# Performance work log

Measured on AMD Instinct MI355X. Metric: run time of the kernel, lower is better.

Reference implementation:

```python
import jax, jax.numpy as jnp
import numpy as np
from jax import lax

B, C, H, W = 8, 1024, 64, 48
A = 9  # anchors per location

def _conv(x, w, b, pad):
    y = lax.conv_general_dilated(x, w, (1, 1), pad,
                                 dimension_numbers=('NCHW', 'OIHW', 'NCHW'))
    return y + b[None, :, None, None]

def setup_inputs() -> dict:
    key = jax.random.key(0)
    ks = jax.random.split(key, 12)
    base_feat = jax.random.normal(ks[0], (B, C, H, W), dtype=jnp.float32)
    W_conv = jax.random.normal(ks[1], (512, C, 3, 3), dtype=jnp.float32) * 0.01
    b_conv = jnp.zeros((512,), jnp.float32)
    W_cls = jax.random.normal(ks[2], (18, 512, 1, 1), dtype=jnp.float32) * 0.01
    b_cls = jnp.zeros((18,), jnp.float32)
    W_bbox = jax.random.normal(ks[3], (36, 512, 1, 1), dtype=jnp.float32) * 0.01
    b_bbox = jnp.zeros((36,), jnp.float32)
    # anchor-target-layer outputs (data-dependent assignment) provided as inputs
    rpn_label = (jax.random.randint(ks[4], (B, A * H * W), 0, 3) - 1).astype(jnp.int32)  # {-1,0,1}
    rpn_bbox_targets = jax.random.normal(ks[5], (B, 36, H, W), dtype=jnp.float32) * 0.1
    rpn_bbox_inside_weights = (jax.random.uniform(ks[6], (B, 36, H, W)) < 0.25).astype(jnp.float32)
    rpn_bbox_outside_weights = jax.random.uniform(ks[7], (B, 36, H, W), dtype=jnp.float32) * 0.01
    return {"base_feat": base_feat, "W_conv": W_conv, "b_conv": b_conv,
            "W_cls": W_cls, "b_cls": b_cls, "W_bbox": W_bbox, "b_bbox": b_bbox,
            "rpn_label": rpn_label, "rpn_bbox_targets": rpn_bbox_targets,
            "rpn_bbox_inside_weights": rpn_bbox_inside_weights,
            "rpn_bbox_outside_weights": rpn_bbox_outside_weights}

def reference(base_feat, W_conv, b_conv, W_cls, b_cls, W_bbox, b_bbox,
              rpn_label, rpn_bbox_targets, rpn_bbox_inside_weights,
              rpn_bbox_outside_weights):
    # RPN head: 3x3 conv + relu, then 1x1 cls / bbox heads
    rpn_conv1 = jax.nn.relu(_conv(base_feat, W_conv, b_conv, ((1, 1), (1, 1))))
    cls_score = _conv(rpn_conv1, W_cls, b_cls, ((0, 0), (0, 0)))   # [B,18,H,W]
    bbox_pred = _conv(rpn_conv1, W_bbox, b_bbox, ((0, 0), (0, 0)))  # [B,36,H,W]
    # reshape to [B,2,A*H,W], softmax over the 2-way fg/bg axis, reshape back
    score_rs = cls_score.reshape(B, 2, A * H, W)
    prob_rs = jax.nn.softmax(score_rs, axis=1)
    rpn_cls_prob = prob_rs.reshape(B, 18, H, W)
    # classification loss: permute(0,2,3,1).view(-1,2), keep labels != -1
    logits = score_rs.transpose(0, 2, 3, 1).reshape(-1, 2)
    label = rpn_label.reshape(-1)
    valid = (label != -1).astype(logits.dtype)
    logp = jax.nn.log_softmax(logits, axis=-1)
    lbl = jnp.clip(label, 0, 1)
    nll = -jnp.take_along_axis(logp, lbl[:, None].astype(jnp.int32), axis=1)[:, 0]
    rpn_loss_cls = jnp.sum(nll * valid) / jnp.maximum(jnp.sum(valid), 1.0)
    # smooth-L1 box loss, sigma=3, summed over dims [1,2,3], mean over batch
    sigma2 = 9.0
    in_diff = rpn_bbox_inside_weights * (bbox_pred - rpn_bbox_targets)
    abs_d = jnp.abs(in_diff)
    sign = lax.stop_gradient((abs_d < 1.0 / sigma2).astype(abs_d.dtype))
    in_loss = in_diff * in_diff * (sigma2 / 2.0) * sign + (abs_d - 0.5 / sigma2) * (1.0 - sign)
    rpn_loss_box = jnp.mean(jnp.sum(rpn_bbox_outside_weights * in_loss, axis=(1, 2, 3)))
    return rpn_cls_prob, bbox_pred, rpn_loss_cls, rpn_loss_box
```

## Files before the change

### kernel.cpp

```cpp
#include <hip/hip_runtime.h>
#include <stdint.h>

#define B_    8
#define CIN   1024
#define H_    64
#define W_    48
#define OC    512
#define HW    3072
#define NPOS  24576
#define K9    9216
#define HP    66
#define WP    50

typedef __attribute__((ext_vector_type(8))) __bf16 bf16x8;
typedef __attribute__((ext_vector_type(4))) float  float4_t;
typedef __attribute__((ext_vector_type(4))) unsigned short ushort4_t;
typedef __attribute__((ext_vector_type(8))) int int8v;
typedef __attribute__((ext_vector_type(4))) int int4v;

__device__ __forceinline__ unsigned short f2bf(float x) {
  union { float f; unsigned u; } v; v.f = x;
  unsigned r = v.u + 0x7FFFu + ((v.u >> 16) & 1u);
  return (unsigned short)(r >> 16);
}

__device__ __forceinline__ unsigned int pack4_fp8(float a, float b, float c, float d) {
  int w = __builtin_amdgcn_cvt_pk_fp8_f32(a, b, 0, false);
  w = __builtin_amdgcn_cvt_pk_fp8_f32(c, d, w, true);
  return (unsigned int)w;
}

__device__ __forceinline__ void async16(const void* g, void* l) {
  __builtin_amdgcn_global_load_lds(
      (const __attribute__((address_space(1))) unsigned int*)g,
      (__attribute__((address_space(3))) unsigned int*)l, 16, 0, 0);
}

__device__ __forceinline__ float wave_sum(float v) {
  for (int o = 32; o > 0; o >>= 1) v += __shfl_down(v, o, 64);
  return v;
}

__global__ void prep_fused(const float* __restrict__ x, const float* __restrict__ Wc,
                           const float* __restrict__ Wcls, const float* __restrict__ Wbb,
                           unsigned char* __restrict__ xt, unsigned char* __restrict__ Wa,
                           unsigned short* __restrict__ Wh, float* __restrict__ accbuf) {
  __shared__ float smem[9216];
  int bid = blockIdx.x, t = threadIdx.x;
  if (bid < 4096) {
    int cx = bid & 7, h = (bid >> 3) & 63, b = bid >> 9;
    float* tile = smem;
    const float* src = x + ((long)(b * CIN + cx * 128) * H_ + h) * W_;
    for (int it = 0; it < 6; ++it) {
      int e = it * 256 + t;
      int cl = e / 12, w4 = e % 12;
      float4_t v = *(const float4_t*)&src[(long)cl * HW + w4 * 4];
      int base = cl * 49 + w4 * 4;
      tile[base] = v.x; tile[base + 1] = v.y; tile[base + 2] = v.z; tile[base + 3] = v.w;
    }
    __syncthreads();
    unsigned char* dst = xt + ((long)(b * HP + h + 1) * WP + 1) * CIN + cx * 128;
    for (int it = 0; it < 6; ++it) {
      int e = it * 256 + t;
      int w = e >> 5, g = e & 31;
      float v0 = tile[(g * 4 + 0) * 49 + w] * 16.f;
      float v1 = tile[(g * 4 + 1) * 49 + w] * 16.f;
      float v2 = tile[(g * 4 + 2) * 49 + w] * 16.f;
      float v3 = tile[(g * 4 + 3) * 49 + w] * 16.f;
      *(unsigned int*)&dst[(long)w * CIN + g * 4] = pack4_fp8(v0, v1, v2, v3);
    }
  } else if (bid < 4608) {
    int o = bid - 4096;
    float* lw = smem;
    const float* src = Wc + (long)o * K9;
    for (int i = 0; i < 9; ++i)
      *(float4_t*)&lw[i * 1024 + t * 4] = *(const float4_t*)&src[i * 1024 + t * 4];
    __syncthreads();
    unsigned char* dst = Wa + (long)o * K9;
    int c = t * 4;
    for (int off = 0; off < 9; ++off) {
      float v0 = lw[(c + 0) * 9 + off] * 512.f;
      float v1 = lw[(c + 1) * 9 + off] * 512.f;
      float v2 = lw[(c + 2) * 9 + off] * 512.f;
      float v3 = lw[(c + 3) * 9 + off] * 512.f;
      *(unsigned int*)&dst[off * 1024 + c] = pack4_fp8(v0, v1, v2, v3);
    }
  } else if (bid < 4640) {
    int e = (bid - 4608) * 1024 + t * 4;
    int m = e >> 9, c = e & 511;
    float v0 = 0.f, v1 = 0.f, v2 = 0.f, v3 = 0.f;
    if (m < 18) {
      const float* s = Wcls + m * 512 + c;
      v0 = s[0]; v1 = s[1]; v2 = s[2]; v3 = s[3];
    } else if (m < 54) {
      const float* s = Wbb + (m - 18) * 512 + c;
      v0 = s[0]; v1 = s[1]; v2 = s[2]; v3 = s[3];
    }
    ushort4_t pk; pk.x = f2bf(v0); pk.y = f2bf(v1); pk.z = f2bf(v2); pk.w = f2bf(v3);
    *(ushort4_t*)&Wh[e] = pk;
    if (bid == 4608 && t < 4) accbuf[t] = 0.f;
  } else {
    int bid2 = bid - 4640;
    int b = bid2 / 66, h = bid2 % 66;
    unsigned char* base = xt + (long)(b * 66 + h) * 50 * 1024;
    int4v z = {};
    if (h == 0 || h == 65) {
      for (int i = t; i < 3200; i += 256) *(int4v*)(base + (long)i * 16) = z;
    } else if (t < 128) {
      int which = t >> 6, off = t & 63;
      *(int4v*)(base + (long)which * 49 * 1024 + (long)off * 16) = z;
    }
  }
}

#define BKF 128
__global__ __launch_bounds__(256, 2)
void conv_gemm(const unsigned char* __restrict__ Wa, const unsigned char* __restrict__ xt,
               const float* __restrict__ bias, unsigned short* __restrict__ conv1) {
  __shared__ unsigned char As[128 * BKF];
  __shared__ unsigned char Bs[128 * BKF];
  int t = threadIdx.x;
  int lane = t & 63, wv = t >> 6;
  int m0 = blockIdx.y * 128;
  int n0 = blockIdx.x * 128;
  const unsigned char* aSrc[4];
  const unsigned char* bSrc[4];
  for (int s = 0; s < 4; ++s) {
    int c = s * 256 + t;
    int r = c >> 3;
    int q = (c & 7) ^ (r & 7);
    aSrc[s] = Wa + (long)(m0 + r) * K9 + q * 16;
    int n = n0 + r; int b = n / HW; int rem = n % HW; int h = rem / W_; int w = rem % W_;
    bSrc[s] = xt + ((long)(b * HP + h) * WP + w) * CIN + q * 16;
  }
  float4_t acc[4][4] = {};
  int wm = wv >> 1, wn = wv & 1;
  int quad = lane >> 4, col = lane & 15;
  for (int kt = 0; kt < 72; ++kt) {
    int off = kt >> 3;
    int dy = off / 3, dx = off % 3;
    long boff = (long)(dy * WP + dx) * CIN + (kt & 7) * 128;
    long aoff = (long)kt * 128;
    __syncthreads();
    for (int s = 0; s < 4; ++s)
      async16(aSrc[s] + aoff, &As[s * 4096 + wv * 1024]);
    for (int s = 0; s < 4; ++s)
      async16(bSrc[s] + boff, &Bs[s * 4096 + wv * 1024]);
    __syncthreads();
    int8v af[4], bfr[4];
    for (int i = 0; i < 4; ++i) {
      int r = wm * 64 + i * 16 + col;
      int rb = r * 128, x7 = r & 7;
      int4v lo = *(const int4v*)&As[rb + (((quad * 2 + 0) ^ x7) << 4)];
      int4v hi = *(const int4v*)&As[rb + (((quad * 2 + 1) ^ x7) << 4)];
      af[i] = (int8v){lo.x, lo.y, lo.z, lo.w, hi.x, hi.y, hi.z, hi.w};
    }
    for (int j = 0; j < 4; ++j) {
      int r = wn * 64 + j * 16 + col;
      int rb = r * 128, x7 = r & 7;
      int4v lo = *(const int4v*)&Bs[rb + (((quad * 2 + 0) ^ x7) << 4)];
      int4v hi = *(const int4v*)&Bs[rb + (((quad * 2 + 1) ^ x7) << 4)];
      bfr[j] = (int8v){lo.x, lo.y, lo.z, lo.w, hi.x, hi.y, hi.z, hi.w};
    }
    for (int i = 0; i < 4; ++i)
      for (int j = 0; j < 4; ++j)
        acc[i][j] = __builtin_amdgcn_mfma_scale_f32_16x16x128_f8f6f4(
            af[i], bfr[j], acc[i][j], 0, 0, 0, 0x76767676, 0, 0x7B7B7B7B);
  }
  for (int i = 0; i < 4; ++i) {
    int mb = m0 + wm * 64 + i * 16 + quad * 4;
    float b0 = bias[mb + 0], b1 = bias[mb + 1], b2 = bias[mb + 2], b3 = bias[mb + 3];
    for (int j = 0; j < 4; ++j) {
      int n = n0 + wn * 64 + j * 16 + col;
      ushort4_t pk;
      pk.x = f2bf(fmaxf(acc[i][j].x + b0, 0.f));
      pk.y = f2bf(fmaxf(acc[i][j].y + b1, 0.f));
      pk.z = f2bf(fmaxf(acc[i][j].z + b2, 0.f));
      pk.w = f2bf(fmaxf(acc[i][j].w + b3, 0.f));
      *(ushort4_t*)&conv1[(long)n * 512 + mb] = pk;
    }
  }
}

__global__ __launch_bounds__(256, 2)
void head_gemm(const unsigned short* __restrict__ Wh, const unsigned short* __restrict__ conv1,
               const float* __restrict__ b_cls, const float* __restrict__ b_bbox,
               float* __restrict__ cls_ws, float* __restrict__ out_bbox) {
  __shared__ unsigned short As[64 * 128];
  __shared__ unsigned short Bs[64 * 128];
  int t = threadIdx.x;
  int lane = t & 63, wv = t >> 6;
  int n0 = blockIdx.x * 64;
  int quad = lane >> 4, col = lane & 15;
  const unsigned short* aS[4];
  const unsigned short* bS[4];
  for (int p = 0; p < 4; ++p) {
    int c = p * 256 + t;
    int r = c >> 4;
    int q = (c & 15) ^ (r & 15);
    aS[p] = Wh + (long)r * 512 + q * 8;
    bS[p] = conv1 + (long)(n0 + r) * 512 + q * 8;
  }
  float4_t acc[4] = {};
  for (int kt = 0; kt < 4; ++kt) {
    long koff = (long)kt * 128;
    __syncthreads();
    for (int p = 0; p < 4; ++p) async16(aS[p] + koff, &As[p * 2048 + wv * 512]);
    for (int p = 0; p < 4; ++p) async16(bS[p] + koff, &Bs[p * 2048 + wv * 512]);
    __syncthreads();
    for (int ks = 0; ks < 4; ++ks) {
      int rn = wv * 16 + col;
      bf16x8 bfr = *(const bf16x8*)&Bs[rn * 128 + (((ks * 4 + quad) ^ (rn & 15)) << 3)];
      for (int i = 0; i < 4; ++i) {
        int r = i * 16 + col;
        bf16x8 af = *(const bf16x8*)&As[r * 128 + (((ks * 4 + quad) ^ (r & 15)) << 3)];
        acc[i] = __builtin_amdgcn_mfma_f32_16x16x32_bf16(af, bfr, acc[i], 0, 0, 0);
      }
    }
  }
  int n = n0 + wv * 16 + col;
  int b = n / HW; int rem = n % HW;
  for (int i = 0; i < 4; ++i) {
    for (int r = 0; r < 4; ++r) {
      int m = i * 16 + quad * 4 + r;
      float v = acc[i][r];
      if (m < 18) {
        cls_ws[(long)(b * 18 + m) * HW + rem] = v + b_cls[m];
      } else if (m < 54) {
        out_bbox[(long)(b * 36 + (m - 18)) * HW + rem] = v + b_bbox[m - 18];
      }
    }
  }
}

__global__ void loss_fused(const float* __restrict__ cls, const int* __restrict__ label,
                           float* __restrict__ prob,
                           const float* __restrict__ pred, const float* __restrict__ tgt,
                           const float* __restrict__ iw, const float* __restrict__ ow,
                           float* __restrict__ acc) {
  int lane = threadIdx.x & 63, wv = threadIdx.x >> 6;
  __shared__ float red[8];
  if (blockIdx.x < 864) {
    int idx = blockIdx.x * 256 + threadIdx.x;
    int b = idx / 27648; int r = idx % 27648;
    int a = r / HW; int r2 = r % HW;
    long i0 = (long)(b * 18 + a) * HW + r2;
    long i1 = i0 + (long)9 * HW;
    float x0 = cls[i0], x1 = cls[i1];
    float mx = fmaxf(x0, x1);
    float e0 = __expf(x0 - mx), e1 = __expf(x1 - mx);
    float s = e0 + e1;
    prob[i0] = e0 / s;
    prob[i1] = e1 / s;
    int lb = label[idx];
    float nll = 0.f, val = 0.f;
    if (lb != -1) {
      val = 1.f;
      float xl = (lb > 0) ? x1 : x0;
      nll = -(xl - mx - __logf(s));
    }
    nll = wave_sum(nll);
    val = wave_sum(val);
    if (lane == 0) { red[wv] = nll; red[4 + wv] = val; }
    __syncthreads();
    if (threadIdx.x == 0) {
      atomicAdd(&acc[0], red[0] + red[1] + red[2] + red[3]);
      atomicAdd(&acc[1], red[4] + red[5] + red[6] + red[7]);
    }
  } else {
    int bid = blockIdx.x - 864;
    float s = 0.f;
    const long total = (long)B_ * 36 * HW;
    for (long i = (long)bid * 256 + threadIdx.x; i < total; i += (long)1728 * 256) {
      float d = iw[i] * (pred[i] - tgt[i]);
      float ad = fabsf(d);
      float l = (ad < (1.f / 9.f)) ? d * d * 4.5f : ad - (1.f / 18.f);
      s += ow[i] * l;
    }
    s = wave_sum(s);
    if (lane == 0) red[wv] = s;
    __syncthreads();
    if (threadIdx.x == 0) atomicAdd(&acc[2], red[0] + red[1] + red[2] + red[3]);
  }
}

__global__ void finalize(const float* __restrict__ acc, float* __restrict__ out) {
  if (threadIdx.x == 0) {
    out[0] = acc[0] / fmaxf(acc[1], 1.f);
    out[1] = acc[2] / (float)B_;
  }
}

extern "C" void kernel_launch(void* const* d_in, const int* in_sizes, int n_in,
                              void* d_out, int out_size, void* d_ws, size_t ws_size,
                              hipStream_t stream) {
  const float* base_feat = (const float*)d_in[0];
  const float* W_conv    = (const float*)d_in[1];
  const float* b_conv    = (const float*)d_in[2];
  const float* W_cls     = (const float*)d_in[3];
  const float* b_cls     = (const float*)d_in[4];
  const float* W_bbox    = (const float*)d_in[5];
  const float* b_bbox    = (const float*)d_in[6];
  const int*   rpn_label = (const int*)d_in[7];
  const float* bb_tgt    = (const float*)d_in[8];
  const float* bb_iw     = (const float*)d_in[9];
  const float* bb_ow     = (const float*)d_in[10];

  float* out = (float*)d_out;
  float* out_cls_prob = out;
  float* out_bbox     = out + 442368;
  float* out_scalars  = out + 442368 + 884736;

  size_t off = 0;
  auto alloc = [&](size_t bytes) {
    void* p = (char*)d_ws + off;
    off = (off + bytes + 255) & ~(size_t)255;
    return p;
  };
  const size_t XT_BYTES = (size_t)B_ * HP * WP * CIN;
  unsigned char*  xt    = (unsigned char*)alloc(XT_BYTES);
  unsigned char*  Wa    = (unsigned char*)alloc((size_t)OC * K9);
  unsigned short* conv1 = (unsigned short*)alloc((size_t)NPOS * OC * 2);
  unsigned short* Wh    = (unsigned short*)alloc((size_t)64 * 512 * 2);
  float* cls_ws         = (float*)alloc((size_t)B_ * 18 * HW * 4);
  float* accbuf         = (float*)alloc(16);

  prep_fused<<<5168, 256, 0, stream>>>(base_feat, W_conv, W_cls, W_bbox, xt, Wa, Wh, accbuf);
  conv_gemm<<<dim3(192, 4), 256, 0, stream>>>(Wa, xt, b_conv, conv1);
  head_gemm<<<384, 256, 0, stream>>>(Wh, conv1, b_cls, b_bbox, cls_ws, out_bbox);
  loss_fused<<<2592, 256, 0, stream>>>(cls_ws, rpn_label, out_cls_prob,
                                       out_bbox, bb_tgt, bb_iw, bb_ow, accbuf);
  finalize<<<1, 64, 0, stream>>>(accbuf, out_scalars);
}
```

Measured before the change: 353.1 us.

## Double-buffer LDS tiles in conv GEMM to overlap async loads with MFMA

```diff
diff --git a/kernel.cpp b/kernel.cpp
--- a/kernel.cpp
+++ b/kernel.cpp
@@ -117,8 +117,8 @@
 __global__ __launch_bounds__(256, 2)
 void conv_gemm(const unsigned char* __restrict__ Wa, const unsigned char* __restrict__ xt,
                const float* __restrict__ bias, unsigned short* __restrict__ conv1) {
-  __shared__ unsigned char As[128 * BKF];
-  __shared__ unsigned char Bs[128 * BKF];
+  __shared__ unsigned char As[2][128 * BKF];
+  __shared__ unsigned char Bs[2][128 * BKF];
   int t = threadIdx.x;
   int lane = t & 63, wv = t >> 6;
   int m0 = blockIdx.y * 128;
@@ -136,37 +136,59 @@
   float4_t acc[4][4] = {};
   int wm = wv >> 1, wn = wv & 1;
   int quad = lane >> 4, col = lane & 15;
-  for (int kt = 0; kt < 72; ++kt) {
+
+  auto stage = [&](int buf, int kt) {
     int off = kt >> 3;
     int dy = off / 3, dx = off % 3;
     long boff = (long)(dy * WP + dx) * CIN + (kt & 7) * 128;
     long aoff = (long)kt * 128;
-    __syncthreads();
     for (int s = 0; s < 4; ++s)
-      async16(aSrc[s] + aoff, &As[s * 4096 + wv * 1024]);
+      async16(aSrc[s] + aoff, &As[buf][s * 4096 + wv * 1024]);
     for (int s = 0; s < 4; ++s)
-      async16(bSrc[s] + boff, &Bs[s * 4096 + wv * 1024]);
-    __syncthreads();
+      async16(bSrc[s] + boff, &Bs[buf][s * 4096 + wv * 1024]);
+  };
+
+  auto compute = [&](int buf) {
     int8v af[4], bfr[4];
     for (int i = 0; i < 4; ++i) {
       int r = wm * 64 + i * 16 + col;
       int rb = r * 128, x7 = r & 7;
-      int4v lo = *(const int4v*)&As[rb + (((quad * 2 + 0) ^ x7) << 4)];
-      int4v hi = *(const int4v*)&As[rb + (((quad * 2 + 1) ^ x7) << 4)];
+      int4v lo = *(const int4v*)&As[buf][rb + (((quad * 2 + 0) ^ x7) << 4)];
+      int4v hi = *(const int4v*)&As[buf][rb + (((quad * 2 + 1) ^ x7) << 4)];
       af[i] = (int8v){lo.x, lo.y, lo.z, lo.w, hi.x, hi.y, hi.z, hi.w};
     }
     for (int j = 0; j < 4; ++j) {
       int r = wn * 64 + j * 16 + col;
       int rb = r * 128, x7 = r & 7;
-      int4v lo = *(const int4v*)&Bs[rb + (((quad * 2 + 0) ^ x7) << 4)];
-      int4v hi = *(const int4v*)&Bs[rb + (((quad * 2 + 1) ^ x7) << 4)];
+      int4v lo = *(const int4v*)&Bs[buf][rb + (((quad * 2 + 0) ^ x7) << 4)];
+      int4v hi = *(const int4v*)&Bs[buf][rb + (((quad * 2 + 1) ^ x7) << 4)];
       bfr[j] = (int8v){lo.x, lo.y, lo.z, lo.w, hi.x, hi.y, hi.z, hi.w};
     }
+    __builtin_amdgcn_s_setprio(1);
     for (int i = 0; i < 4; ++i)
       for (int j = 0; j < 4; ++j)
         acc[i][j] = __builtin_amdgcn_mfma_scale_f32_16x16x128_f8f6f4(
             af[i], bfr[j], acc[i][j], 0, 0, 0, 0x76767676, 0, 0x7B7B7B7B);
-  }
+    __builtin_amdgcn_s_setprio(0);
+    __builtin_amdgcn_sched_barrier(0);
+    asm volatile("s_waitcnt lgkmcnt(0)\n\ts_barrier" ::: "memory");
+  };
+
+  stage(0, 0);
+#pragma unroll 1
+  for (int kt = 0; kt < 72; kt += 2) {
+    stage(1, kt + 1);
+    asm volatile("s_waitcnt vmcnt(8)\n\ts_barrier" ::: "memory");
+    compute(0);
+    if (kt + 2 < 72) {
+      stage(0, kt + 2);
+      asm volatile("s_waitcnt vmcnt(8)\n\ts_barrier" ::: "memory");
+    } else {
+      asm volatile("s_waitcnt vmcnt(0)\n\ts_barrier" ::: "memory");
+    }
+    compute(1);
+  }
+
   for (int i = 0; i < 4; ++i) {
     int mb = m0 + wm * 64 + i * 16 + quad * 4;
     float b0 = bias[mb + 0], b1 = bias[mb + 1], b2 = bias[mb + 2], b3 = bias[mb + 3];
```

Result: slower. 374.2 us (+6.0%).
